# Kernel tuning notes

Measured on AMD Instinct MI355X. Metric: run time of the kernel, lower is better.

The kernel has to match this reference:

```python
import math
import jax, jax.numpy as jnp
import numpy as np

B, S, HID, NH = 1, 2048, 4096, 32
HD = HID // NH  # 128
INV_NORM = 1.0 / math.sqrt(HD)


def _build_alibi(n_heads, seq_len, batch):
    # Standard Bloom ALiBi slopes.
    cp2 = 2 ** math.floor(math.log2(n_heads))
    base = 2.0 ** (-(2.0 ** -(math.log2(cp2) - 3)))
    slopes = base ** np.arange(1, cp2 + 1)
    if cp2 != n_heads:
        extra_base = 2.0 ** (-(2.0 ** -(math.log2(2 * cp2) - 3)))
        n_rem = min(cp2, n_heads - cp2)
        slopes = np.concatenate([slopes, extra_base ** np.arange(1, 2 * n_rem + 1, 2)])
    arange = np.arange(seq_len, dtype=np.float32)[None, None, :]
    alibi = slopes[:, None, None].astype(np.float32) * arange  # [NH,1,S]
    alibi = np.broadcast_to(alibi[None], (batch, n_heads, 1, seq_len)).reshape(batch * n_heads, 1, seq_len)
    return jnp.asarray(alibi, jnp.float32)


def setup_inputs() -> dict:
    key = jax.random.key(0)
    ks = jax.random.split(key, 5)
    return {
        "hidden_states": jax.random.normal(ks[0], (B, S, HID), jnp.float32),
        "alibi": _build_alibi(NH, S, B),  # [B*NH, 1, S]
        "w_qkv": jax.random.normal(ks[1], (3 * HID, HID), jnp.float32) * 0.02,
        "b_qkv": jax.random.normal(ks[2], (3 * HID,), jnp.float32) * 0.02,
        "w_dense": jax.random.normal(ks[3], (HID, HID), jnp.float32) * 0.02,
        "b_dense": jax.random.normal(ks[4], (HID,), jnp.float32) * 0.02,
    }


def reference(hidden_states, alibi, w_qkv, b_qkv, w_dense, b_dense):
    b, s, _ = hidden_states.shape
    # Fused QKV projection, per-head interleaved layout [B,S,NH,3,HD]
    fused = hidden_states @ w_qkv.T + b_qkv
    fused = fused.reshape(b, s, NH, 3, HD)
    q = fused[..., 0, :].transpose(0, 2, 1, 3).reshape(b * NH, s, HD)
    k = fused[..., 1, :].transpose(0, 2, 1, 3).reshape(b * NH, s, HD)
    v = fused[..., 2, :].transpose(0, 2, 1, 3).reshape(b * NH, s, HD)
    # baddbmm(alibi, q, k^T, beta=1.0, alpha=inv_norm_factor)
    scores = alibi + INV_NORM * jnp.einsum("bqd,bkd->bqk", q, k)  # [B*NH,S,S]
    causal = jnp.tril(jnp.ones((s, s), dtype=bool))
    scores = jnp.where(causal[None], scores, jnp.finfo(scores.dtype).min)
    probs = jax.nn.softmax(scores.astype(jnp.float32), axis=-1).astype(hidden_states.dtype)
    ctx = jnp.einsum("bqk,bkd->bqd", probs, v)  # [B*NH,S,HD]
    ctx = ctx.reshape(b, NH, s, HD).transpose(0, 2, 1, 3).reshape(b, s, HID)
    return ctx @ w_dense.T + b_dense
```

## Files before the change

kernel.cpp:

```cpp
#include <hip/hip_runtime.h>
#include <math.h>


typedef __attribute__((ext_vector_type(8))) short short8;
typedef __attribute__((ext_vector_type(4))) float floatx4;
typedef __attribute__((ext_vector_type(4))) unsigned short ushort4v;

#define S_LEN 2048
#define HID_DIM 4096
#define NHEADS 32
#define HDIM 128
#define QKV_N 12288
#define QK_STRIDE 8192
#define INV_NORM 0.08838834764831845f

__device__ __forceinline__ unsigned short f2bf(float f) {
    union { float f; unsigned int i; } v; v.f = f;
    unsigned int u = v.i;
    return (unsigned short)((u + 0x7fffu + ((u >> 16) & 1u)) >> 16);
}

typedef __attribute__((address_space(1))) unsigned int guint;
typedef __attribute__((address_space(3))) unsigned int luint;
__device__ __forceinline__ void gl_lds16(const unsigned short* g, unsigned short* l) {
    __builtin_amdgcn_global_load_lds((guint*)g, (luint*)l, 16, 0, 0);
}

__global__ __launch_bounds__(256) void cvt_bf16(
    const float* __restrict__ src, unsigned short* __restrict__ dst)
{
    size_t i = ((size_t)blockIdx.x * 256 + threadIdx.x) * 8;
    float4 x = *(const float4*)(src + i);
    float4 y = *(const float4*)(src + i + 4);
    union { unsigned u[4]; short8 s; } r;
    r.u[0] = (unsigned)f2bf(x.x) | ((unsigned)f2bf(x.y) << 16);
    r.u[1] = (unsigned)f2bf(x.z) | ((unsigned)f2bf(x.w) << 16);
    r.u[2] = (unsigned)f2bf(y.x) | ((unsigned)f2bf(y.y) << 16);
    r.u[3] = (unsigned)f2bf(y.z) | ((unsigned)f2bf(y.w) << 16);
    *(short8*)(dst + i) = r.s;
}

template <int MODE>
__global__ __launch_bounds__(256) void gemm_bt(
    const unsigned short* __restrict__ A,
    const unsigned short* __restrict__ B,
    const float* __restrict__ bias,
    unsigned short* __restrict__ Cq,
    float* __restrict__ Cf,
    unsigned short* __restrict__ vt,
    int M, int N, int K)
{
    __shared__ unsigned short a_lds[128 * 64];
    __shared__ unsigned short b_lds[128 * 64];
    int t = threadIdx.x;
    int w = t >> 6, lane = t & 63, quad = lane >> 4, l15 = lane & 15;
    int mb = blockIdx.y * 128, nb = blockIdx.x * 128;
    int wm = (w >> 1) * 64, wn = (w & 1) * 64;

    int lr = lane >> 3;
    int lcol = ((lane & 7) ^ lr) * 8;
    const unsigned short* pa = A + (size_t)(mb + w * 32 + lr) * K + lcol;
    const unsigned short* pb = B + (size_t)(nb + w * 32 + lr) * K + lcol;
    unsigned short* la = &a_lds[(w * 32) * 64];
    unsigned short* lb = &b_lds[(w * 32) * 64];

    floatx4 acc[4][4];
    for (int i = 0; i < 4; i++)
        for (int j = 0; j < 4; j++) acc[i][j] = (floatx4)0.0f;

    for (int k0 = 0; k0 < K; k0 += 64) {
        for (int it = 0; it < 4; it++) {
            gl_lds16(pa + k0 + (size_t)it * 8 * K, la + it * 8 * 64);
            gl_lds16(pb + k0 + (size_t)it * 8 * K, lb + it * 8 * 64);
        }
        __syncthreads();
        for (int ks = 0; ks < 2; ks++) {
            short8 af[4], bfr[4];
            for (int i = 0; i < 4; i++) {
                int r = wm + i * 16 + l15;
                af[i] = *(const short8*)&a_lds[r * 64 + (((ks * 4 + quad) ^ (l15 & 7)) * 8)];
            }
            for (int j = 0; j < 4; j++) {
                int r = wn + j * 16 + l15;
                bfr[j] = *(const short8*)&b_lds[r * 64 + (((ks * 4 + quad) ^ (l15 & 7)) * 8)];
            }
            for (int i = 0; i < 4; i++)
                for (int j = 0; j < 4; j++)
                    acc[i][j] = __builtin_amdgcn_mfma_f32_16x16x32_bf16(af[i], bfr[j], acc[i][j], 0, 0, 0);
        }
        __syncthreads();
    }

    if (MODE == 1) {
        int type = blockIdx.x % 3;
        int h = blockIdx.x / 3;
        if (type == 2) {
            for (int j = 0; j < 4; j++) {
                int local = wn + j * 16 + l15;
                float bv = bias[nb + local];
                unsigned short* vp = vt + ((size_t)h * HDIM + local) * S_LEN;
                for (int i = 0; i < 4; i++) {
                    int rowbase = mb + wm + i * 16 + quad * 4;
                    ushort4v pk;
                    for (int r = 0; r < 4; r++) pk[r] = f2bf(acc[i][j][r] + bv);
                    *(ushort4v*)&vp[rowbase] = pk;
                }
            }
        } else {
            size_t colbase = (size_t)h * 256 + type * 128;
            for (int j = 0; j < 4; j++) {
                int local = wn + j * 16 + l15;
                float bv = bias[nb + local];
                for (int i = 0; i < 4; i++) {
                    int rowbase = mb + wm + i * 16 + quad * 4;
                    for (int r = 0; r < 4; r++)
                        Cq[(size_t)(rowbase + r) * QK_STRIDE + colbase + local] =
                            f2bf(acc[i][j][r] + bv);
                }
            }
        }
    } else {
        for (int j = 0; j < 4; j++) {
            int col = nb + wn + j * 16 + l15;
            float bv = bias[col];
            for (int i = 0; i < 4; i++) {
                int rowbase = mb + wm + i * 16 + quad * 4;
                for (int r = 0; r < 4; r++)
                    Cf[(size_t)(rowbase + r) * N + col] = acc[i][j][r] + bv;
            }
        }
    }
}

__global__ __launch_bounds__(256) void attn_flash(
    const unsigned short* __restrict__ qk,
    const unsigned short* __restrict__ vt,
    const float* __restrict__ alibi,
    unsigned short* __restrict__ ctx)
{
    __shared__ unsigned short k_lds[64 * 136];
    __shared__ unsigned short vt_lds[128 * 72];
    __shared__ unsigned short p_lds[4 * 16 * 72];

    int h = blockIdx.x;
    int qb = blockIdx.y * 64;
    int t = threadIdx.x;
    int w = t >> 6, lane = t & 63, quad = lane >> 4, l15 = lane & 15;
    int qoff = h * 256;

    short8 qf[4];
    {
        int qrow = qb + w * 16 + l15;
        const unsigned short* qp = qk + (size_t)qrow * QK_STRIDE + qoff;
        for (int ks = 0; ks < 4; ks++)
            qf[ks] = *(const short8*)&qp[ks * 32 + quad * 8];
    }

    floatx4 o[8];
    for (int j = 0; j < 8; j++) o[j] = (floatx4)0.0f;
    float m_prev[4], l_prev[4];
    for (int r = 0; r < 4; r++) { m_prev[r] = -INFINITY; l_prev[r] = 0.0f; }

    int ntiles = qb / 64 + 1;
    for (int tile = 0; tile < ntiles; tile++) {
        int kb = tile * 64;
        for (int i = 0; i < 4; i++) {
            int idx = t + 256 * i;
            int krow = idx >> 4, kcol = (idx & 15) * 8;
            *(short8*)&k_lds[krow * 136 + kcol] =
                *(const short8*)(qk + (size_t)(kb + krow) * QK_STRIDE + qoff + 128 + kcol);
            int d = idx >> 3, ch = (idx & 7) * 8;
            *(short8*)&vt_lds[d * 72 + ch] =
                *(const short8*)(vt + ((size_t)h * HDIM + d) * S_LEN + kb + ch);
        }
        __syncthreads();

        floatx4 s[4];
        for (int j = 0; j < 4; j++) s[j] = (floatx4)0.0f;
        for (int ks = 0; ks < 4; ks++) {
            for (int j = 0; j < 4; j++) {
                short8 bfr = *(const short8*)&k_lds[(j * 16 + l15) * 136 + ks * 32 + quad * 8];
                s[j] = __builtin_amdgcn_mfma_f32_16x16x32_bf16(qf[ks], bfr, s[j], 0, 0, 0);
            }
        }

        float sv[4][4];
        for (int j = 0; j < 4; j++) {
            int kcol = kb + j * 16 + l15;
            float al = alibi[h * S_LEN + kcol];
            for (int r = 0; r < 4; r++) {
                int qrow = qb + w * 16 + quad * 4 + r;
                float x = s[j][r] * INV_NORM + al;
                sv[j][r] = (kcol <= qrow) ? x : -INFINITY;
            }
        }

        float p[4][4];
        for (int r = 0; r < 4; r++) {
            float mt = fmaxf(fmaxf(sv[0][r], sv[1][r]), fmaxf(sv[2][r], sv[3][r]));
            for (int off = 1; off < 16; off <<= 1)
                mt = fmaxf(mt, __shfl_xor(mt, off, 64));
            float m_new = fmaxf(m_prev[r], mt);
            float alpha = __expf(m_prev[r] - m_new);
            float rs = 0.0f;
            for (int j = 0; j < 4; j++) {
                float pv = __expf(sv[j][r] - m_new);
                p[j][r] = pv;
                rs += pv;
            }
            for (int off = 1; off < 16; off <<= 1)
                rs += __shfl_xor(rs, off, 64);
            l_prev[r] = l_prev[r] * alpha + rs;
            m_prev[r] = m_new;
            for (int j = 0; j < 8; j++) o[j][r] *= alpha;
        }

        {
            unsigned short* pb = &p_lds[w * 16 * 72];
            for (int j = 0; j < 4; j++)
                for (int r = 0; r < 4; r++)
                    pb[(quad * 4 + r) * 72 + j * 16 + l15] = f2bf(p[j][r]);
        }
        {
            const unsigned short* pb = &p_lds[w * 16 * 72];
            for (int ks = 0; ks < 2; ks++) {
                short8 ap = *(const short8*)&pb[l15 * 72 + ks * 32 + quad * 8];
                for (int j = 0; j < 8; j++) {
                    short8 bv = *(const short8*)&vt_lds[(j * 16 + l15) * 72 + ks * 32 + quad * 8];
                    o[j] = __builtin_amdgcn_mfma_f32_16x16x32_bf16(ap, bv, o[j], 0, 0, 0);
                }
            }
        }
        __syncthreads();
    }

    for (int r = 0; r < 4; r++) {
        float linv = 1.0f / l_prev[r];
        int qrow = qb + w * 16 + quad * 4 + r;
        unsigned short* op = ctx + (size_t)qrow * HID_DIM + h * HDIM;
        for (int j = 0; j < 8; j++)
            op[j * 16 + l15] = f2bf(o[j][r] * linv);
    }
}

extern "C" void kernel_launch(void* const* d_in, const int* in_sizes, int n_in,
                              void* d_out, int out_size, void* d_ws, size_t ws_size,
                              hipStream_t stream) {
    const float* hidden  = (const float*)d_in[0];
    const float* alibi   = (const float*)d_in[1];
    const float* w_qkv   = (const float*)d_in[2];
    const float* b_qkv   = (const float*)d_in[3];
    const float* w_dense = (const float*)d_in[4];
    const float* b_dense = (const float*)d_in[5];
    float* out = (float*)d_out;

    unsigned short* ws    = (unsigned short*)d_ws;
    unsigned short* wq_bf = ws;
    unsigned short* fused = ws + (size_t)50331648;
    unsigned short* vt    = fused + (size_t)S_LEN * QK_STRIDE;
    unsigned short* hbf   = vt + (size_t)NHEADS * HDIM * S_LEN;
    unsigned short* ctx   = hbf;
    unsigned short* wd_bf = wq_bf;

    dim3 blk(256);
    cvt_bf16<<<dim3(4096),  blk, 0, stream>>>(hidden,  hbf);
    cvt_bf16<<<dim3(24576), blk, 0, stream>>>(w_qkv,   wq_bf);
    gemm_bt<1><<<dim3(QKV_N / 128, S_LEN / 128), blk, 0, stream>>>(
        hbf, wq_bf, b_qkv, fused, nullptr, vt, S_LEN, QKV_N, HID_DIM);
    attn_flash<<<dim3(NHEADS, S_LEN / 64), blk, 0, stream>>>(fused, vt, alibi, ctx);
    cvt_bf16<<<dim3(8192), blk, 0, stream>>>(w_dense, wd_bf);
    gemm_bt<0><<<dim3(HID_DIM / 128, S_LEN / 128), blk, 0, stream>>>(
        ctx, wd_bf, b_dense, nullptr, out, nullptr, S_LEN, HID_DIM, HID_DIM);
}
```

Baseline: 850.6 us.

## Use 32x32 MFMA in GEMMs and restructure attention to skip LDS staging

The GEMM kernel switches from 16x16x32 to 32x32x16 bf16 MFMA with a 2x2 accumulator layout per wave, which cuts LDS fragment reads per MFMA. The attention kernel drops shared-memory staging of K and V and the block barriers, reading fragments straight from global memory. It also computes the softmax row sum with an extra MFMA against a ones vector instead of shuffles, applies the causal mask only on the diagonal tile, and swaps the grid order so consecutive blocks share a head. The attention changes trade LDS traffic and synchronisation for uncoalesced, cache-dependent global loads.

```diff
diff --git a/kernel.cpp b/kernel.cpp
--- a/kernel.cpp
+++ b/kernel.cpp
@@ -4,6 +4,7 @@
 
 typedef __attribute__((ext_vector_type(8))) short short8;
 typedef __attribute__((ext_vector_type(4))) float floatx4;
+typedef __attribute__((ext_vector_type(16))) float floatx16;
 typedef __attribute__((ext_vector_type(4))) unsigned short ushort4v;
 
 #define S_LEN 2048
@@ -53,20 +54,21 @@
     __shared__ unsigned short a_lds[128 * 64];
     __shared__ unsigned short b_lds[128 * 64];
     int t = threadIdx.x;
-    int w = t >> 6, lane = t & 63, quad = lane >> 4, l15 = lane & 15;
+    int w = t >> 6, lane = t & 63;
+    int l31 = lane & 31, half = lane >> 5, l7 = lane & 7;
     int mb = blockIdx.y * 128, nb = blockIdx.x * 128;
     int wm = (w >> 1) * 64, wn = (w & 1) * 64;
 
     int lr = lane >> 3;
-    int lcol = ((lane & 7) ^ lr) * 8;
+    int lcol = (l7 ^ lr) * 8;
     const unsigned short* pa = A + (size_t)(mb + w * 32 + lr) * K + lcol;
     const unsigned short* pb = B + (size_t)(nb + w * 32 + lr) * K + lcol;
     unsigned short* la = &a_lds[(w * 32) * 64];
     unsigned short* lb = &b_lds[(w * 32) * 64];
 
-    floatx4 acc[4][4];
-    for (int i = 0; i < 4; i++)
-        for (int j = 0; j < 4; j++) acc[i][j] = (floatx4)0.0f;
+    floatx16 acc[2][2];
+    for (int i = 0; i < 2; i++)
+        for (int j = 0; j < 2; j++) acc[i][j] = (floatx16)0.0f;
 
     for (int k0 = 0; k0 < K; k0 += 64) {
         for (int it = 0; it < 4; it++) {
@@ -74,19 +76,20 @@
             gl_lds16(pb + k0 + (size_t)it * 8 * K, lb + it * 8 * 64);
         }
         __syncthreads();
-        for (int ks = 0; ks < 2; ks++) {
-            short8 af[4], bfr[4];
-            for (int i = 0; i < 4; i++) {
-                int r = wm + i * 16 + l15;
-                af[i] = *(const short8*)&a_lds[r * 64 + (((ks * 4 + quad) ^ (l15 & 7)) * 8)];
-            }
-            for (int j = 0; j < 4; j++) {
-                int r = wn + j * 16 + l15;
-                bfr[j] = *(const short8*)&b_lds[r * 64 + (((ks * 4 + quad) ^ (l15 & 7)) * 8)];
-            }
-            for (int i = 0; i < 4; i++)
-                for (int j = 0; j < 4; j++)
-                    acc[i][j] = __builtin_amdgcn_mfma_f32_16x16x32_bf16(af[i], bfr[j], acc[i][j], 0, 0, 0);
+        for (int ks = 0; ks < 4; ks++) {
+            int chunk = ks * 2 + half;
+            short8 af[2], bfr[2];
+            for (int i = 0; i < 2; i++) {
+                int r = wm + i * 32 + l31;
+                af[i] = *(const short8*)&a_lds[r * 64 + ((chunk ^ (r & 7)) * 8)];
+            }
+            for (int j = 0; j < 2; j++) {
+                int r = wn + j * 32 + l31;
+                bfr[j] = *(const short8*)&b_lds[r * 64 + ((chunk ^ (r & 7)) * 8)];
+            }
+            for (int i = 0; i < 2; i++)
+                for (int j = 0; j < 2; j++)
+                    acc[i][j] = __builtin_amdgcn_mfma_f32_32x32x16_bf16(af[i], bfr[j], acc[i][j], 0, 0, 0);
         }
         __syncthreads();
     }
@@ -95,39 +98,42 @@
         int type = blockIdx.x % 3;
         int h = blockIdx.x / 3;
         if (type == 2) {
-            for (int j = 0; j < 4; j++) {
-                int local = wn + j * 16 + l15;
+            for (int j = 0; j < 2; j++) {
+                int local = wn + j * 32 + l31;
                 float bv = bias[nb + local];
                 unsigned short* vp = vt + ((size_t)h * HDIM + local) * S_LEN;
-                for (int i = 0; i < 4; i++) {
-                    int rowbase = mb + wm + i * 16 + quad * 4;
-                    ushort4v pk;
-                    for (int r = 0; r < 4; r++) pk[r] = f2bf(acc[i][j][r] + bv);
-                    *(ushort4v*)&vp[rowbase] = pk;
-                }
+                for (int i = 0; i < 2; i++)
+                    for (int g = 0; g < 4; g++) {
+                        int rowbase = mb + wm + i * 32 + g * 8 + 4 * half;
+                        ushort4v pk;
+                        for (int r = 0; r < 4; r++) pk[r] = f2bf(acc[i][j][g * 4 + r] + bv);
+                        *(ushort4v*)&vp[rowbase] = pk;
+                    }
             }
         } else {
             size_t colbase = (size_t)h * 256 + type * 128;
-            for (int j = 0; j < 4; j++) {
-                int local = wn + j * 16 + l15;
+            for (int j = 0; j < 2; j++) {
+                int local = wn + j * 32 + l31;
                 float bv = bias[nb + local];
-                for (int i = 0; i < 4; i++) {
-                    int rowbase = mb + wm + i * 16 + quad * 4;
+                for (int i = 0; i < 2; i++)
+                    for (int g = 0; g < 4; g++) {
+                        int rowbase = mb + wm + i * 32 + g * 8 + 4 * half;
+                        for (int r = 0; r < 4; r++)
+                            Cq[(size_t)(rowbase + r) * QK_STRIDE + colbase + local] =
+                                f2bf(acc[i][j][g * 4 + r] + bv);
+                    }
+            }
+        }
+    } else {
+        for (int j = 0; j < 2; j++) {
+            int col = nb + wn + j * 32 + l31;
+            float bv = bias[col];
+            for (int i = 0; i < 2; i++)
+                for (int g = 0; g < 4; g++) {
+                    int rowbase = mb + wm + i * 32 + g * 8 + 4 * half;
                     for (int r = 0; r < 4; r++)
-                        Cq[(size_t)(rowbase + r) * QK_STRIDE + colbase + local] =
-                            f2bf(acc[i][j][r] + bv);
+                        Cf[(size_t)(rowbase + r) * N + col] = acc[i][j][g * 4 + r] + bv;
                 }
-            }
-        }
-    } else {
-        for (int j = 0; j < 4; j++) {
-            int col = nb + wn + j * 16 + l15;
-            float bv = bias[col];
-            for (int i = 0; i < 4; i++) {
-                int rowbase = mb + wm + i * 16 + quad * 4;
-                for (int r = 0; r < 4; r++)
-                    Cf[(size_t)(rowbase + r) * N + col] = acc[i][j][r] + bv;
-            }
         }
     }
 }
@@ -138,52 +144,51 @@
     const float* __restrict__ alibi,
     unsigned short* __restrict__ ctx)
 {
-    __shared__ unsigned short k_lds[64 * 136];
-    __shared__ unsigned short vt_lds[128 * 72];
     __shared__ unsigned short p_lds[4 * 16 * 72];
 
-    int h = blockIdx.x;
-    int qb = blockIdx.y * 64;
+    int qtile = blockIdx.x, h = blockIdx.y;
+    int qb = qtile * 64;
     int t = threadIdx.x;
     int w = t >> 6, lane = t & 63, quad = lane >> 4, l15 = lane & 15;
     int qoff = h * 256;
 
     short8 qf[4];
     {
-        int qrow = qb + w * 16 + l15;
-        const unsigned short* qp = qk + (size_t)qrow * QK_STRIDE + qoff;
+        const unsigned short* qp = qk + (size_t)(qb + w * 16 + l15) * QK_STRIDE + qoff;
         for (int ks = 0; ks < 4; ks++)
             qf[ks] = *(const short8*)&qp[ks * 32 + quad * 8];
     }
 
-    floatx4 o[8];
+    const unsigned short* kbase = qk + qoff + 128 + (size_t)l15 * QK_STRIDE + quad * 8;
+    const unsigned short* vbase = vt + ((size_t)h * HDIM + l15) * S_LEN + quad * 8;
+
+    short8 ones;
+    {
+        union { unsigned u[4]; short8 s; } ov;
+        unsigned ob = (l15 == 0) ? 0x3F803F80u : 0u;
+        ov.u[0] = ob; ov.u[1] = ob; ov.u[2] = ob; ov.u[3] = ob;
+        ones = ov.s;
+    }
+
+    floatx4 o[8], o8;
     for (int j = 0; j < 8; j++) o[j] = (floatx4)0.0f;
-    float m_prev[4], l_prev[4];
-    for (int r = 0; r < 4; r++) { m_prev[r] = -INFINITY; l_prev[r] = 0.0f; }
-
-    int ntiles = qb / 64 + 1;
+    o8 = (floatx4)0.0f;
+    float m_prev[4];
+    for (int r = 0; r < 4; r++) m_prev[r] = -INFINITY;
+
+    int ntiles = qtile + 1;
     for (int tile = 0; tile < ntiles; tile++) {
         int kb = tile * 64;
-        for (int i = 0; i < 4; i++) {
-            int idx = t + 256 * i;
-            int krow = idx >> 4, kcol = (idx & 15) * 8;
-            *(short8*)&k_lds[krow * 136 + kcol] =
-                *(const short8*)(qk + (size_t)(kb + krow) * QK_STRIDE + qoff + 128 + kcol);
-            int d = idx >> 3, ch = (idx & 7) * 8;
-            *(short8*)&vt_lds[d * 72 + ch] =
-                *(const short8*)(vt + ((size_t)h * HDIM + d) * S_LEN + kb + ch);
-        }
-        __syncthreads();
-
         floatx4 s[4];
         for (int j = 0; j < 4; j++) s[j] = (floatx4)0.0f;
-        for (int ks = 0; ks < 4; ks++) {
+        const unsigned short* kt = kbase + (size_t)kb * QK_STRIDE;
+        for (int ks = 0; ks < 4; ks++)
             for (int j = 0; j < 4; j++) {
-                short8 bfr = *(const short8*)&k_lds[(j * 16 + l15) * 136 + ks * 32 + quad * 8];
+                short8 bfr = *(const short8*)(kt + (size_t)j * 16 * QK_STRIDE + ks * 32);
                 s[j] = __builtin_amdgcn_mfma_f32_16x16x32_bf16(qf[ks], bfr, s[j], 0, 0, 0);
             }
-        }
-
+
+        bool last = (tile == ntiles - 1);
         float sv[4][4];
         for (int j = 0; j < 4; j++) {
             int kcol = kb + j * 16 + l15;
@@ -191,7 +196,7 @@
             for (int r = 0; r < 4; r++) {
                 int qrow = qb + w * 16 + quad * 4 + r;
                 float x = s[j][r] * INV_NORM + al;
-                sv[j][r] = (kcol <= qrow) ? x : -INFINITY;
+                sv[j][r] = (!last || kcol <= qrow) ? x : -INFINITY;
             }
         }
 
@@ -202,40 +207,32 @@
                 mt = fmaxf(mt, __shfl_xor(mt, off, 64));
             float m_new = fmaxf(m_prev[r], mt);
             float alpha = __expf(m_prev[r] - m_new);
-            float rs = 0.0f;
-            for (int j = 0; j < 4; j++) {
-                float pv = __expf(sv[j][r] - m_new);
-                p[j][r] = pv;
-                rs += pv;
-            }
-            for (int off = 1; off < 16; off <<= 1)
-                rs += __shfl_xor(rs, off, 64);
-            l_prev[r] = l_prev[r] * alpha + rs;
+            for (int j = 0; j < 4; j++)
+                p[j][r] = __expf(sv[j][r] - m_new);
             m_prev[r] = m_new;
             for (int j = 0; j < 8; j++) o[j][r] *= alpha;
-        }
-
-        {
-            unsigned short* pb = &p_lds[w * 16 * 72];
-            for (int j = 0; j < 4; j++)
-                for (int r = 0; r < 4; r++)
-                    pb[(quad * 4 + r) * 72 + j * 16 + l15] = f2bf(p[j][r]);
-        }
-        {
-            const unsigned short* pb = &p_lds[w * 16 * 72];
-            for (int ks = 0; ks < 2; ks++) {
-                short8 ap = *(const short8*)&pb[l15 * 72 + ks * 32 + quad * 8];
-                for (int j = 0; j < 8; j++) {
-                    short8 bv = *(const short8*)&vt_lds[(j * 16 + l15) * 72 + ks * 32 + quad * 8];
-                    o[j] = __builtin_amdgcn_mfma_f32_16x16x32_bf16(ap, bv, o[j], 0, 0, 0);
-                }
-            }
-        }
-        __syncthreads();
+            o8[r] *= alpha;
+        }
+
+        unsigned short* pb = &p_lds[w * 16 * 72];
+        for (int j = 0; j < 4; j++)
+            for (int r = 0; r < 4; r++)
+                pb[(quad * 4 + r) * 72 + j * 16 + l15] = f2bf(p[j][r]);
+
+        const unsigned short* vtb = vbase + kb;
+        for (int ks = 0; ks < 2; ks++) {
+            short8 ap = *(const short8*)&pb[l15 * 72 + ks * 32 + quad * 8];
+            for (int j = 0; j < 8; j++) {
+                short8 bv = *(const short8*)(vtb + (size_t)j * 16 * S_LEN + ks * 32);
+                o[j] = __builtin_amdgcn_mfma_f32_16x16x32_bf16(ap, bv, o[j], 0, 0, 0);
+            }
+            o8 = __builtin_amdgcn_mfma_f32_16x16x32_bf16(ap, ones, o8, 0, 0, 0);
+        }
     }
 
     for (int r = 0; r < 4; r++) {
-        float linv = 1.0f / l_prev[r];
+        float l = __shfl(o8[r], 0, 16);
+        float linv = 1.0f / l;
         int qrow = qb + w * 16 + quad * 4 + r;
         unsigned short* op = ctx + (size_t)qrow * HID_DIM + h * HDIM;
         for (int j = 0; j < 8; j++)
@@ -267,7 +264,7 @@
     cvt_bf16<<<dim3(24576), blk, 0, stream>>>(w_qkv,   wq_bf);
     gemm_bt<1><<<dim3(QKV_N / 128, S_LEN / 128), blk, 0, stream>>>(
         hbf, wq_bf, b_qkv, fused, nullptr, vt, S_LEN, QKV_N, HID_DIM);
-    attn_flash<<<dim3(NHEADS, S_LEN / 64), blk, 0, stream>>>(fused, vt, alibi, ctx);
+    attn_flash<<<dim3(S_LEN / 64, NHEADS), blk, 0, stream>>>(fused, vt, alibi, ctx);
     cvt_bf16<<<dim3(8192), blk, 0, stream>>>(w_dense, wd_bf);
     gemm_bt<0><<<dim3(HID_DIM / 128, S_LEN / 128), blk, 0, stream>>>(
         ctx, wd_bf, b_dense, nullptr, out, nullptr, S_LEN, HID_DIM, HID_DIM);
```

After: 1.366 ms. 60.6% more time.
